# Performance work log

Measured on AMD Instinct MI355X. Metric: run time of the kernel, lower is better.

Reference implementation:

```python
import jax, jax.numpy as jnp
import numpy as np

VOCAB = 26 + 26 + 10 + 3  # 65
EMBED = 6
HIDDEN = EMBED + 1  # class vector + accumulator


def setup_inputs() -> dict:
    key = jax.random.key(0)
    ks = jax.random.split(key, 8)
    B, T = 2048, 1024
    x = jax.random.randint(ks[0], (B, T), 0, VOCAB, dtype=jnp.int64)
    embed = jax.random.normal(ks[1], (VOCAB, EMBED), dtype=jnp.float32)
    hidden_init = jax.random.normal(ks[2], (1, HIDDEN), dtype=jnp.float32)
    reset_threshold = jax.random.normal(ks[3], (1,), dtype=jnp.float32)
    temperature = jnp.asarray(0.01, dtype=jnp.float32)
    class_transition = jax.random.normal(ks[4], (EMBED, EMBED), dtype=jnp.float32)
    reset_transition = jax.random.normal(ks[5], (EMBED, EMBED), dtype=jnp.float32)
    output = jax.random.normal(ks[6], (EMBED, VOCAB), dtype=jnp.float32)
    return {
        "x": x,
        "embed": embed,
        "hidden_init": hidden_init,
        "reset_threshold": reset_threshold,
        "temperature": temperature,
        "class_transition": class_transition,
        "reset_transition": reset_transition,
        "output": output,
    }


def reference(x, embed, hidden_init, reset_threshold, temperature,
              class_transition, reset_transition, output):
    B, T = x.shape
    e = embed[x]  # [B, T, E] embedding lookup
    h0 = jnp.broadcast_to(hidden_init, (B, HIDDEN))

    thr2 = reset_threshold ** 2  # scalar-shaped [1]

    def cell(hidden, x_t):
        # hidden: [B, 7]; x_t: [B, 6]
        expected_class = hidden[:, :-1]          # [B, 6]
        prev_accum = hidden[:, -1:]              # [B, 1]
        # batched dot product x_t . expected_class -> [B, 1]
        similarity = jnp.sum(x_t * expected_class, axis=-1, keepdims=True)
        addition = jax.nn.relu((1.0 + prev_accum) * similarity) - prev_accum
        new_accum = prev_accum + addition
        reset = jax.nn.sigmoid((new_accum - thr2) / temperature)  # [B, 1]
        next_accum = (1.0 - reset) * new_accum
        transition_class = x_t @ class_transition   # [B, 6]
        reset_class = x_t @ reset_transition        # [B, 6]
        next_class = reset * reset_class + (1.0 - reset) * transition_class
        new_hidden = jnp.concatenate([next_class, next_accum], axis=1)  # [B, 7]
        return new_hidden, new_hidden

    # scan over time: carry hidden state, collect all hiddens
    _, hs = jax.lax.scan(cell, h0, jnp.swapaxes(e, 0, 1))  # hs: [T, B, 7]
    hidden_states = jnp.swapaxes(hs, 0, 1)                 # [B, T, 7]
    output_logits = hidden_states[:, :, :-1] @ output      # [B, T, VOCAB]
    return output_logits
```

## Files before the change

### kernel.cpp

```cpp
#include <hip/hip_runtime.h>

#define TV 65
#define NB 2048
#define NT 1024

typedef float f32x4 __attribute__((ext_vector_type(4)));

#define OFF_SP 0
#define OFF_LP 8450
#define OFF_S0 16900
#define OFF_R  17792

__global__ __launch_bounds__(256) void k_build(
    const float* __restrict__ embed, const float* __restrict__ ct,
    const float* __restrict__ rt, const float* __restrict__ hinit,
    const float* __restrict__ outw, float* __restrict__ ws) {
  __shared__ float tc_s[TV][6];
  __shared__ float rc_s[TV][6];
  int v = threadIdx.x;
  if (v < TV) {
    float e[6];
#pragma unroll
    for (int k = 0; k < 6; k++) e[k] = embed[v * 6 + k];
#pragma unroll
    for (int j = 0; j < 6; j++) {
      float stc = 0.f, src = 0.f;
#pragma unroll
      for (int k = 0; k < 6; k++) {
        stc += e[k] * ct[k * 6 + j];
        src += e[k] * rt[k * 6 + j];
      }
      tc_s[v][j] = stc;
      rc_s[v][j] = src;
    }
    float s0 = 0.f;
#pragma unroll
    for (int k = 0; k < 6; k++) s0 += e[k] * hinit[k];
    ws[OFF_S0 + v] = s0;
  }
  __syncthreads();
  for (int idx = threadIdx.x; idx < 2 * 4225; idx += 256) {
    int tbl = idx / 4225;
    int e2 = idx - tbl * 4225;
    int a = e2 / 65;
    int b = e2 - a * 65;
    if (tbl == 0) {
      float stc = 0.f, src = 0.f;
#pragma unroll
      for (int k = 0; k < 6; k++) {
        stc += embed[a * 6 + k] * tc_s[b][k];
        src += embed[a * 6 + k] * rc_s[b][k];
      }
      ((float2*)(ws + OFF_SP))[e2] = make_float2(stc, src);
    } else {
      float ltc = 0.f, lrc = 0.f;
#pragma unroll
      for (int k = 0; k < 6; k++) {
        ltc += tc_s[a][k] * outw[k * 65 + b];
        lrc += rc_s[a][k] * outw[k * 65 + b];
      }
      ((float2*)(ws + OFF_LP))[e2] = make_float2(ltc, lrc);
    }
  }
}

__global__ __launch_bounds__(256) void k_rnn_spec(
    const int* __restrict__ x, float* __restrict__ ws,
    const float* __restrict__ thr, const float* __restrict__ temp,
    const float* __restrict__ hinit) {
  __shared__ float2 sSP[4225];
  const float2* __restrict__ gSP = (const float2*)(ws + OFF_SP);
  for (int i = threadIdx.x; i < 4225; i += 256) sSP[i] = gSP[i];
  __syncthreads();

  const int tid = blockIdx.x * 256 + threadIdx.x;
  const int c = tid >> 11;
  const int row = tid & 2047;
  const int t0 = c * 32;
  int s0 = t0 - 96;
  if (s0 < 0) s0 = 0;
  const bool exact = (s0 == 0);
  const int NG = (t0 + 32 - s0) >> 2;

  const float t0v = thr[0];
  const float thr2 = t0v * t0v;
  const float invtemp = 1.0f / temp[0];
  const int* xp = x + row * NT;
  float* rbase = ws + OFF_R + row * NT;

  int4 xa = *(const int4*)(xp + s0);
  int4 xb = *(const int4*)(xp + s0 + 4);
  int4 xc = *(const int4*)(xp + s0 + 8);
  int4 xd = *(const int4*)(xp + s0 + 12);

  float pa, r_prev, omr_prev;
  float2 sp0;
  if (exact) {
    float s0v = ws[OFF_S0 + xa.x];
    sp0 = make_float2(s0v, s0v);
    pa = hinit[6];
    r_prev = 0.5f;
    omr_prev = 0.5f;
  } else {
    int vm1 = xp[s0 - 1];
    sp0 = sSP[xa.x * 65 + vm1];
    pa = 0.0f;
    r_prev = 1.0f;
    omr_prev = 0.0f;
  }
  float2 sp1 = sSP[xa.y * 65 + xa.x];
  float2 sp2 = sSP[xa.z * 65 + xa.y];
  float2 sp3 = sSP[xa.w * 65 + xa.z];

#define STEP(SP, ROUT)                               \
  {                                                  \
    float sim = r_prev * (SP).y + omr_prev * (SP).x; \
    float prod = (1.0f + pa) * sim;                  \
    float aa = fmaxf(prod, 0.0f);                    \
    float add = aa - pa;                             \
    float na = pa + add;                             \
    float p = __expf((thr2 - na) * invtemp);         \
    float r = __builtin_amdgcn_rcpf(1.0f + p);       \
    float omr = 1.0f - r;                            \
    pa = omr * na;                                   \
    r_prev = r;                                      \
    omr_prev = omr;                                  \
    ROUT = r;                                        \
  }

  for (int g = 0; g < NG; ++g) {
    int offn = s0 + 4 * (g + 4);
    if (offn > NT - 4) offn = s0;
    int4 xe = *(const int4*)(xp + offn);
    float2 n0 = sSP[xb.x * 65 + xa.w];
    float2 n1 = sSP[xb.y * 65 + xb.x];
    float2 n2 = sSP[xb.z * 65 + xb.y];
    float2 n3 = sSP[xb.w * 65 + xb.z];

    float4 rq;
    STEP(sp0, rq.x);
    STEP(sp1, rq.y);
    STEP(sp2, rq.z);
    STEP(sp3, rq.w);
    int st = s0 + 4 * g;
    if (st >= t0) *(float4*)(rbase + st) = rq;

    sp0 = n0; sp1 = n1; sp2 = n2; sp3 = n3;
    xa = xb; xb = xc; xc = xd; xd = xe;
  }
#undef STEP
}

#define NF4 34078720u
#define PSTRIDE 524288u
__global__ __launch_bounds__(256) void k_proj(
    const int* __restrict__ x, const float* __restrict__ ws,
    float* __restrict__ out) {
  __shared__ float2 sLP[4225];
  const float2* __restrict__ gLP = (const float2*)(ws + OFF_LP);
  for (int i = threadIdx.x; i < 4225; i += 256) sLP[i] = gLP[i];
  __syncthreads();

  unsigned gid = blockIdx.x * 256u + threadIdx.x;
  for (unsigned i4 = gid; i4 < NF4; i4 += PSTRIDE) {
    unsigned base = i4 * 4u;
    unsigned n = base / 65u;
    unsigned v = base - n * 65u;
    unsigned n1 = n + 1u;
    if (n1 > 2097151u) n1 = 2097151u;
    int xv = x[n];
    int xv2 = x[n1];
    float r = ws[OFF_R + n];
    float r2 = ws[OFF_R + n1];
    float omr = 1.0f - r;
    float omr2 = 1.0f - r2;
    unsigned offA = (unsigned)xv * 65u + v;
    unsigned offB = (unsigned)xv2 * 65u + v - 65u;
    f32x4 o;
#pragma unroll
    for (int j = 0; j < 4; ++j) {
      bool wrap = (v + (unsigned)j) >= 65u;
      unsigned off = (wrap ? offB : offA) + (unsigned)j;
      float2 p = sLP[off];
      float rr = wrap ? r2 : r;
      float oo = wrap ? omr2 : omr;
      o[j] = rr * p.y + oo * p.x;
    }
    *(f32x4*)(out + base) = o;
  }
}

extern "C" void kernel_launch(void* const* d_in, const int* in_sizes, int n_in,
                              void* d_out, int out_size, void* d_ws, size_t ws_size,
                              hipStream_t stream) {
  const int* x = (const int*)d_in[0];
  const float* embed = (const float*)d_in[1];
  const float* hinit = (const float*)d_in[2];
  const float* thr = (const float*)d_in[3];
  const float* temp = (const float*)d_in[4];
  const float* ct = (const float*)d_in[5];
  const float* rt = (const float*)d_in[6];
  const float* outw = (const float*)d_in[7];
  float* ws = (float*)d_ws;
  float* out = (float*)d_out;

  hipLaunchKernelGGL(k_build, dim3(1), dim3(256), 0, stream, embed, ct, rt, hinit, outw, ws);
  hipLaunchKernelGGL(k_rnn_spec, dim3(256), dim3(256), 0, stream, x, ws, thr, temp, hinit);
  hipLaunchKernelGGL(k_proj, dim3(2048), dim3(256), 0, stream, x, ws, out);
}
```

Baseline: 166.0 us.

## Fuse reset-scan and output projection into one kernel with LDS-resident per-row state

Merges the speculative RNN reset-computation kernel and the projection kernel into a single kernel, where each block handles 4 rows. It stages the tokens as bytes in shared memory and keeps the reset values in LDS instead of writing them to global workspace and reading them back. Only 128 threads per block run the sequential scan while the rest sit idle. The pair table is then swapped for the logit table in the same LDS buffer and the block writes its own output slice. This removes one launch and a global round-trip for the reset values. In exchange, the scan phase runs at reduced parallelism (512x128 threads) and the projection cannot overlap with other blocks' scans except across blocks.

```diff
diff --git a/kernel.cpp b/kernel.cpp
--- a/kernel.cpp
+++ b/kernel.cpp
@@ -9,7 +9,6 @@
 #define OFF_SP 0
 #define OFF_LP 8450
 #define OFF_S0 16900
-#define OFF_R  17792
 
 __global__ __launch_bounds__(256) void k_build(
     const float* __restrict__ embed, const float* __restrict__ ct,
@@ -64,53 +63,65 @@
   }
 }
 
-__global__ __launch_bounds__(256) void k_rnn_spec(
-    const int* __restrict__ x, float* __restrict__ ws,
+__global__ __launch_bounds__(256) void k_fused(
+    const int* __restrict__ x, const float* __restrict__ ws,
     const float* __restrict__ thr, const float* __restrict__ temp,
-    const float* __restrict__ hinit) {
-  __shared__ float2 sSP[4225];
+    const float* __restrict__ hinit, float* __restrict__ out) {
+  __shared__ float2 sTab[4225];
+  __shared__ float r_s[4 * 1024];
+  __shared__ unsigned char x_s[4 * 1024];
+
+  const int b = blockIdx.x;
+  const int t = threadIdx.x;
+
+  const int* xg = x + b * 4096;
+  for (int i = t; i < 1024; i += 256) {
+    int4 xv4 = ((const int4*)xg)[i];
+    ((uchar4*)x_s)[i] = make_uchar4((unsigned char)xv4.x, (unsigned char)xv4.y,
+                                    (unsigned char)xv4.z, (unsigned char)xv4.w);
+  }
   const float2* __restrict__ gSP = (const float2*)(ws + OFF_SP);
-  for (int i = threadIdx.x; i < 4225; i += 256) sSP[i] = gSP[i];
-  __syncthreads();
-
-  const int tid = blockIdx.x * 256 + threadIdx.x;
-  const int c = tid >> 11;
-  const int row = tid & 2047;
-  const int t0 = c * 32;
-  int s0 = t0 - 96;
-  if (s0 < 0) s0 = 0;
-  const bool exact = (s0 == 0);
-  const int NG = (t0 + 32 - s0) >> 2;
-
-  const float t0v = thr[0];
-  const float thr2 = t0v * t0v;
-  const float invtemp = 1.0f / temp[0];
-  const int* xp = x + row * NT;
-  float* rbase = ws + OFF_R + row * NT;
-
-  int4 xa = *(const int4*)(xp + s0);
-  int4 xb = *(const int4*)(xp + s0 + 4);
-  int4 xc = *(const int4*)(xp + s0 + 8);
-  int4 xd = *(const int4*)(xp + s0 + 12);
-
-  float pa, r_prev, omr_prev;
-  float2 sp0;
-  if (exact) {
-    float s0v = ws[OFF_S0 + xa.x];
-    sp0 = make_float2(s0v, s0v);
-    pa = hinit[6];
-    r_prev = 0.5f;
-    omr_prev = 0.5f;
-  } else {
-    int vm1 = xp[s0 - 1];
-    sp0 = sSP[xa.x * 65 + vm1];
-    pa = 0.0f;
-    r_prev = 1.0f;
-    omr_prev = 0.0f;
-  }
-  float2 sp1 = sSP[xa.y * 65 + xa.x];
-  float2 sp2 = sSP[xa.z * 65 + xa.y];
-  float2 sp3 = sSP[xa.w * 65 + xa.z];
+  for (int i = t; i < 4225; i += 256) sTab[i] = gSP[i];
+  __syncthreads();
+
+  if (t < 128) {
+    const int chunk = t & 31;
+    const int row_loc = t >> 5;
+    const int t0 = chunk * 32;
+    int s0 = t0 - 96;
+    if (s0 < 0) s0 = 0;
+    const bool exact = (s0 == 0);
+    const int NG = (t0 + 32 - s0) >> 2;
+
+    const float t0v = thr[0];
+    const float thr2 = t0v * t0v;
+    const float invtemp = 1.0f / temp[0];
+    const unsigned char* xp = x_s + row_loc * 1024;
+    float* rp = r_s + row_loc * 1024;
+
+    unsigned tw = *(const unsigned*)(xp + s0);
+    unsigned a0 = tw & 255u, a1 = (tw >> 8) & 255u;
+    unsigned a2 = (tw >> 16) & 255u, a3 = tw >> 24;
+
+    float pa, r_prev, omr_prev;
+    float2 sp0;
+    if (exact) {
+      float s0v = ws[OFF_S0 + a0];
+      sp0 = make_float2(s0v, s0v);
+      pa = hinit[6];
+      r_prev = 0.5f;
+      omr_prev = 0.5f;
+    } else {
+      unsigned vm1 = xp[s0 - 1];
+      sp0 = sTab[a0 * 65 + vm1];
+      pa = 0.0f;
+      r_prev = 1.0f;
+      omr_prev = 0.0f;
+    }
+    float2 sp1 = sTab[a1 * 65 + a0];
+    float2 sp2 = sTab[a2 * 65 + a1];
+    float2 sp3 = sTab[a3 * 65 + a2];
+    unsigned last = a3;
 
 #define STEP(SP, ROUT)                               \
   {                                                  \
@@ -128,65 +139,60 @@
     ROUT = r;                                        \
   }
 
-  for (int g = 0; g < NG; ++g) {
-    int offn = s0 + 4 * (g + 4);
-    if (offn > NT - 4) offn = s0;
-    int4 xe = *(const int4*)(xp + offn);
-    float2 n0 = sSP[xb.x * 65 + xa.w];
-    float2 n1 = sSP[xb.y * 65 + xb.x];
-    float2 n2 = sSP[xb.z * 65 + xb.y];
-    float2 n3 = sSP[xb.w * 65 + xb.z];
-
-    float4 rq;
-    STEP(sp0, rq.x);
-    STEP(sp1, rq.y);
-    STEP(sp2, rq.z);
-    STEP(sp3, rq.w);
-    int st = s0 + 4 * g;
-    if (st >= t0) *(float4*)(rbase + st) = rq;
-
-    sp0 = n0; sp1 = n1; sp2 = n2; sp3 = n3;
-    xa = xb; xb = xc; xc = xd; xd = xe;
-  }
+    for (int g = 0; g < NG; ++g) {
+      int offn = s0 + 4 * (g + 1);
+      if (offn > NT - 4) offn = s0;
+      unsigned twn = *(const unsigned*)(xp + offn);
+      unsigned b0 = twn & 255u, b1 = (twn >> 8) & 255u;
+      unsigned b2 = (twn >> 16) & 255u, b3 = twn >> 24;
+      float2 n0 = sTab[b0 * 65 + last];
+      float2 n1v = sTab[b1 * 65 + b0];
+      float2 n2 = sTab[b2 * 65 + b1];
+      float2 n3 = sTab[b3 * 65 + b2];
+
+      float4 rq;
+      STEP(sp0, rq.x);
+      STEP(sp1, rq.y);
+      STEP(sp2, rq.z);
+      STEP(sp3, rq.w);
+      int st = s0 + 4 * g;
+      if (st >= t0) *(float4*)(rp + st) = rq;
+
+      sp0 = n0; sp1 = n1v; sp2 = n2; sp3 = n3;
+      last = b3;
+    }
 #undef STEP
-}
-
-#define NF4 34078720u
-#define PSTRIDE 524288u
-__global__ __launch_bounds__(256) void k_proj(
-    const int* __restrict__ x, const float* __restrict__ ws,
-    float* __restrict__ out) {
-  __shared__ float2 sLP[4225];
+  }
+  __syncthreads();
+
   const float2* __restrict__ gLP = (const float2*)(ws + OFF_LP);
-  for (int i = threadIdx.x; i < 4225; i += 256) sLP[i] = gLP[i];
-  __syncthreads();
-
-  unsigned gid = blockIdx.x * 256u + threadIdx.x;
-  for (unsigned i4 = gid; i4 < NF4; i4 += PSTRIDE) {
+  for (int i = t; i < 4225; i += 256) sTab[i] = gLP[i];
+  __syncthreads();
+
+  float* ob = out + (size_t)b * 266240u;
+  for (unsigned i4 = t; i4 < 66560u; i4 += 256u) {
     unsigned base = i4 * 4u;
     unsigned n = base / 65u;
     unsigned v = base - n * 65u;
-    unsigned n1 = n + 1u;
-    if (n1 > 2097151u) n1 = 2097151u;
-    int xv = x[n];
-    int xv2 = x[n1];
-    float r = ws[OFF_R + n];
-    float r2 = ws[OFF_R + n1];
-    float omr = 1.0f - r;
-    float omr2 = 1.0f - r2;
-    unsigned offA = (unsigned)xv * 65u + v;
-    unsigned offB = (unsigned)xv2 * 65u + v - 65u;
+    unsigned n1i = n + 1u;
+    if (n1i > 4095u) n1i = 4095u;
+    unsigned xv = x_s[n];
+    unsigned xv2 = x_s[n1i];
+    float r = r_s[n], r2 = r_s[n1i];
+    float omr = 1.0f - r, omr2 = 1.0f - r2;
+    unsigned offA = xv * 65u + v;
+    unsigned offB = xv2 * 65u + v - 65u;
     f32x4 o;
 #pragma unroll
     for (int j = 0; j < 4; ++j) {
       bool wrap = (v + (unsigned)j) >= 65u;
       unsigned off = (wrap ? offB : offA) + (unsigned)j;
-      float2 p = sLP[off];
+      float2 p = sTab[off];
       float rr = wrap ? r2 : r;
       float oo = wrap ? omr2 : omr;
       o[j] = rr * p.y + oo * p.x;
     }
-    *(f32x4*)(out + base) = o;
+    *(f32x4*)(ob + base) = o;
   }
 }
 
@@ -205,6 +211,5 @@
   float* out = (float*)d_out;
 
   hipLaunchKernelGGL(k_build, dim3(1), dim3(256), 0, stream, embed, ct, rt, hinit, outw, ws);
-  hipLaunchKernelGGL(k_rnn_spec, dim3(256), dim3(256), 0, stream, x, ws, thr, temp, hinit);
-  hipLaunchKernelGGL(k_proj, dim3(2048), dim3(256), 0, stream, x, ws, out);
+  hipLaunchKernelGGL(k_fused, dim3(512), dim3(256), 0, stream, x, ws, thr, temp, hinit, out);
 }
```

New measurement: 141.3 us. 14.9% less time.

## Stage token ids and reset gates in shared memory for output projection

Applied to the files above, without the earlier changes.

The projection kernel now gives each block a contiguous 64K-float slice of the output. It preloads the needed token ids (as bytes) and reset values into shared memory, and each thread writes 16 consecutive floats per iteration. The logit table now stores the difference between the reset and transition logits, so each output needs one FMA instead of two multiplies. The aim is to remove redundant global reads of x and r and the per-element division. The cost is a less coalesced store pattern and more registers.

```diff
diff --git a/kernel.cpp b/kernel.cpp
--- a/kernel.cpp
+++ b/kernel.cpp
@@ -3,6 +3,7 @@
 #define TV 65
 #define NB 2048
 #define NT 1024
+#define NTOK 2097152u
 
 typedef float f32x4 __attribute__((ext_vector_type(4)));
 
@@ -59,7 +60,7 @@
         ltc += tc_s[a][k] * outw[k * 65 + b];
         lrc += rc_s[a][k] * outw[k * 65 + b];
       }
-      ((float2*)(ws + OFF_LP))[e2] = make_float2(ltc, lrc);
+      ((float2*)(ws + OFF_LP))[e2] = make_float2(ltc, lrc - ltc);
     }
   }
 }
@@ -151,42 +152,61 @@
 #undef STEP
 }
 
-#define NF4 34078720u
-#define PSTRIDE 524288u
 __global__ __launch_bounds__(256) void k_proj(
     const int* __restrict__ x, const float* __restrict__ ws,
     float* __restrict__ out) {
   __shared__ float2 sLP[4225];
+  __shared__ float r_s[1016];
+  __shared__ unsigned char x_s[1016];
+  const unsigned b = blockIdx.x, t = threadIdx.x;
+  const unsigned F0 = b * 65536u;
+  const unsigned n0 = F0 / 65u;
+
   const float2* __restrict__ gLP = (const float2*)(ws + OFF_LP);
-  for (int i = threadIdx.x; i < 4225; i += 256) sLP[i] = gLP[i];
+  for (unsigned i = t; i < 4225u; i += 256u) sLP[i] = gLP[i];
+  for (unsigned i = t; i < 1016u; i += 256u) {
+    unsigned n = n0 + i;
+    if (n > NTOK - 1u) n = NTOK - 1u;
+    x_s[i] = (unsigned char)x[n];
+    r_s[i] = ws[OFF_R + n];
+  }
   __syncthreads();
 
-  unsigned gid = blockIdx.x * 256u + threadIdx.x;
-  for (unsigned i4 = gid; i4 < NF4; i4 += PSTRIDE) {
-    unsigned base = i4 * 4u;
-    unsigned n = base / 65u;
-    unsigned v = base - n * 65u;
-    unsigned n1 = n + 1u;
-    if (n1 > 2097151u) n1 = 2097151u;
-    int xv = x[n];
-    int xv2 = x[n1];
-    float r = ws[OFF_R + n];
-    float r2 = ws[OFF_R + n1];
-    float omr = 1.0f - r;
-    float omr2 = 1.0f - r2;
-    unsigned offA = (unsigned)xv * 65u + v;
-    unsigned offB = (unsigned)xv2 * 65u + v - 65u;
-    f32x4 o;
-#pragma unroll
-    for (int j = 0; j < 4; ++j) {
-      bool wrap = (v + (unsigned)j) >= 65u;
-      unsigned off = (wrap ? offB : offA) + (unsigned)j;
-      float2 p = sLP[off];
-      float rr = wrap ? r2 : r;
-      float oo = wrap ? omr2 : omr;
-      o[j] = rr * p.y + oo * p.x;
-    }
-    *(f32x4*)(out + base) = o;
+  unsigned F = F0 + t * 16u;
+  unsigned n = F / 65u;
+  unsigned v = F - n * 65u;
+  unsigned nl = n - n0;
+  for (int it = 0; it < 16; ++it) {
+    unsigned k = 65u - v;
+    unsigned xv = x_s[nl];
+    float rA = r_s[nl];
+    unsigned xv2 = x_s[nl + 1u];
+    float rB = r_s[nl + 1u];
+    unsigned idxA = xv * 65u + v;
+    unsigned idxB = xv2 * 65u - k;
+    float oo[16];
+#pragma unroll
+    for (unsigned e = 0; e < 16u; ++e) {
+      bool inA = e < k;
+      unsigned idx = (inA ? idxA : idxB) + e;
+      float2 p = sLP[idx];
+      float rr = inA ? rA : rB;
+      oo[e] = fmaf(rr, p.y, p.x);
+    }
+#pragma unroll
+    for (int g4 = 0; g4 < 4; ++g4) {
+      f32x4 q;
+      q.x = oo[4 * g4 + 0];
+      q.y = oo[4 * g4 + 1];
+      q.z = oo[4 * g4 + 2];
+      q.w = oo[4 * g4 + 3];
+      *(f32x4*)(out + F + 4 * g4) = q;
+    }
+    F += 4096u;
+    v += 1u;
+    unsigned w = (v == 65u) ? 1u : 0u;
+    nl += 63u + w;
+    v = w ? 0u : v;
   }
 }
 
@@ -206,5 +226,5 @@
 
   hipLaunchKernelGGL(k_build, dim3(1), dim3(256), 0, stream, embed, ct, rt, hinit, outw, ws);
   hipLaunchKernelGGL(k_rnn_spec, dim3(256), dim3(256), 0, stream, x, ws, thr, temp, hinit);
-  hipLaunchKernelGGL(k_proj, dim3(2048), dim3(256), 0, stream, x, ws, out);
-}
+  hipLaunchKernelGGL(k_proj, dim3(2080), dim3(256), 0, stream, x, ws, out);
+}
```

Result: slower. 214.5 us (+29.2%).
